# Performance work log

Measured on AMD Instinct MI355X. Metric: run time of the kernel, lower is better.

The kernel has to match this reference:

```python
import jax, jax.numpy as jnp
import numpy as np

N_NODES = 100000


def _aggregate(features, edge_index, edge_weight):
    # weighted scatter-add over edges + degree normalization (clamped at 1)
    src = edge_index[0]
    dst = edge_index[1]
    w = edge_weight  # [E]
    msgs = features[src] * w[:, None]                      # [E, D]
    agg = jax.ops.segment_sum(msgs, dst, num_segments=N_NODES)   # [N, D]
    deg = jax.ops.segment_sum(w, dst, num_segments=N_NODES)      # [N]
    deg = jnp.maximum(deg, 1.0)
    return agg / deg[:, None]


def setup_inputs() -> dict:
    key = jax.random.key(0)
    k1, k2, k3, k4, k5, k6, k7, k8, k9 = jax.random.split(key, 9)
    input_dim, hidden_dim, embedding_dim, num_classes = 128, 128, 64, 40
    E = 1600000
    node_features = jax.random.normal(k1, (N_NODES, input_dim), dtype=jnp.float32)
    edge_index = jax.random.randint(k2, (2, E), 0, N_NODES, dtype=jnp.int64)
    edge_weight = jax.random.uniform(k3, (E,), dtype=jnp.float32)
    s1 = 1.0 / np.sqrt(input_dim)
    s2 = 1.0 / np.sqrt(hidden_dim)
    s3 = 1.0 / np.sqrt(embedding_dim)
    W1 = jax.random.uniform(k4, (hidden_dim, input_dim), minval=-s1, maxval=s1, dtype=jnp.float32)
    b1 = jax.random.uniform(k5, (hidden_dim,), minval=-s1, maxval=s1, dtype=jnp.float32)
    W2 = jax.random.uniform(k6, (embedding_dim, hidden_dim), minval=-s2, maxval=s2, dtype=jnp.float32)
    b2 = jax.random.uniform(k7, (embedding_dim,), minval=-s2, maxval=s2, dtype=jnp.float32)
    W3 = jax.random.uniform(k8, (num_classes, embedding_dim), minval=-s3, maxval=s3, dtype=jnp.float32)
    b3 = jax.random.uniform(k9, (num_classes,), minval=-s3, maxval=s3, dtype=jnp.float32)
    return {"node_features": node_features, "edge_index": edge_index, "edge_weight": edge_weight,
            "W1": W1, "b1": b1, "W2": W2, "b2": b2, "W3": W3, "b3": b3}


def reference(node_features, edge_index, edge_weight, W1, b1, W2, b2, W3, b3):
    hidden = _aggregate(node_features, edge_index, edge_weight)
    hidden = jax.nn.relu(hidden @ W1.T + b1)
    embedding = _aggregate(hidden, edge_index, edge_weight) @ W2.T + b2
    logits = embedding @ W3.T + b3
    return (embedding, logits)
```

## Files before the change

### kernel.cpp

```cpp
#include <hip/hip_runtime.h>
#include <cstddef>

#define DIM 128
#define DH 64
#define NC 40
#define NBLKA 1024
#define BKT 512

typedef short bf16x8 __attribute__((ext_vector_type(8)));
typedef float f32x4  __attribute__((ext_vector_type(4)));

__device__ __forceinline__ unsigned short f2bf(float f) {
    unsigned int u = __float_as_uint(f);
    u += 0x7FFFu + ((u >> 16) & 1u);
    return (unsigned short)(u >> 16);
}
__device__ __forceinline__ float bf2f(unsigned short h) {
    return __uint_as_float(((unsigned int)h) << 16);
}

__global__ __launch_bounds__(256) void kA1(
    const int* __restrict__ dstv, int E, int CHUNK,
    int* __restrict__ cnt , int NBbkt,
    const float* __restrict__ W1, const float* __restrict__ W2,
    unsigned short* __restrict__ W1bf, unsigned short* __restrict__ W2bf)
{
    int b = blockIdx.x;
    if (b < NBLKA) {
        __shared__ int h[256];
        for (int i = threadIdx.x; i < 256; i += 256) h[i] = 0;
        __syncthreads();
        int lo = b * CHUNK, hi = min(E, lo + CHUNK);
        for (int e = lo + threadIdx.x; e < hi; e += 256)
            atomicAdd(&h[dstv[e] >> 9], 1);
        __syncthreads();
        for (int i = threadIdx.x; i < NBbkt; i += 256)
            cnt[(size_t)b * NBbkt + i] = h[i];
    } else {
        int i = (b - NBLKA) * 256 + threadIdx.x;
        if (i < DIM * DIM) W1bf[i] = f2bf(W1[i]);
        else if (i < DIM * DIM + DH * DIM) {
            int j = i - DIM * DIM;
            W2bf[j] = f2bf(W2[j]);
        }
    }
}

__global__ __launch_bounds__(256) void kA2a(
    int* __restrict__ cnt , int* __restrict__ total, int NBbkt)
{
    __shared__ int wsum[4];
    int b = blockIdx.x;
    int t = threadIdx.x;
    int v[4]; int s = 0;
    #pragma unroll
    for (int i = 0; i < 4; ++i) { v[i] = cnt[(size_t)(4 * t + i) * NBbkt + b]; s += v[i]; }
    int lane = t & 63, wv = t >> 6;
    int si = s;
    #pragma unroll
    for (int off = 1; off < 64; off <<= 1) {
        int x = __shfl_up(si, off);
        if (lane >= off) si += x;
    }
    if (lane == 63) wsum[wv] = si;
    __syncthreads();
    int wbase = 0;
    for (int i = 0; i < wv; ++i) wbase += wsum[i];
    int run = wbase + si - s;
    #pragma unroll
    for (int i = 0; i < 4; ++i) { cnt[(size_t)(4 * t + i) * NBbkt + b] = run; run += v[i]; }
    if (t == 255) total[b] = run;
}

__global__ __launch_bounds__(256) void kA2b(
    const int* __restrict__ total, int* __restrict__ bucketBase, int NBbkt)
{
    __shared__ int wsum[4];
    int t = threadIdx.x;
    int v = (t < NBbkt) ? total[t] : 0;
    int lane = t & 63, wv = t >> 6;
    int si = v;
    #pragma unroll
    for (int off = 1; off < 64; off <<= 1) {
        int x = __shfl_up(si, off);
        if (lane >= off) si += x;
    }
    if (lane == 63) wsum[wv] = si;
    __syncthreads();
    int wbase = 0;
    for (int i = 0; i < wv; ++i) wbase += wsum[i];
    int incl = wbase + si;
    if (t < NBbkt) bucketBase[t + 1] = incl;
    if (t == 0) bucketBase[0] = 0;
}

__global__ __launch_bounds__(256) void kA3(
    const int* __restrict__ srcv, const int* __restrict__ dstv,
    const float* __restrict__ wv_, int E, int CHUNK,
    const int* __restrict__ exclOff, const int* __restrict__ bucketBase,
    uint2* __restrict__ staging, int NBbkt,
    const float4* __restrict__ feat4, ushort4* __restrict__ featbf4, int n8)
{
    int b = blockIdx.x;
    if (b < NBLKA) {
        __shared__ int cur[256];
        for (int i = threadIdx.x; i < NBbkt; i += 256)
            cur[i] = bucketBase[i] + exclOff[(size_t)b * NBbkt + i];
        __syncthreads();
        int lo = b * CHUNK, hi = min(E, lo + CHUNK);
        for (int e = lo + threadIdx.x; e < hi; e += 256) {
            int d = dstv[e];
            unsigned q = (unsigned)(wv_[e] * 32767.f + 0.5f);
            unsigned word = (q << 17) | (unsigned)srcv[e];
            int pos = atomicAdd(&cur[d >> 9], 1);
            staging[pos] = make_uint2(word, (unsigned)(d & (BKT - 1)));
        }
    } else {
        int i = (b - NBLKA) * 256 + threadIdx.x;
        if (i < n8) {
            float4 x = feat4[2 * i], y = feat4[2 * i + 1];
            ushort4 o1, o2;
            o1.x = f2bf(x.x); o1.y = f2bf(x.y); o1.z = f2bf(x.z); o1.w = f2bf(x.w);
            o2.x = f2bf(y.x); o2.y = f2bf(y.y); o2.z = f2bf(y.z); o2.w = f2bf(y.w);
            featbf4[2 * i] = o1; featbf4[2 * i + 1] = o2;
        }
    }
}

__global__ __launch_bounds__(256) void kB(
    const uint2* __restrict__ staging, const int* __restrict__ bucketBase,
    unsigned* __restrict__ csr, int* __restrict__ row_start, int n)
{
    __shared__ int bins[BKT];
    __shared__ int cur[BKT];
    __shared__ int wsum[4];
    int b = blockIdx.x;
    int base = bucketBase[b], cntE = bucketBase[b + 1] - base;
    int t = threadIdx.x;
    for (int i = t; i < BKT; i += 256) bins[i] = 0;
    __syncthreads();
    for (int i = t; i < cntE; i += 256)
        atomicAdd(&bins[staging[base + i].y], 1);
    __syncthreads();
    int b0 = bins[2 * t], b1 = bins[2 * t + 1];
    int s = b0 + b1;
    int lane = t & 63, wv = t >> 6;
    int si = s;
    #pragma unroll
    for (int off = 1; off < 64; off <<= 1) {
        int x = __shfl_up(si, off);
        if (lane >= off) si += x;
    }
    if (lane == 63) wsum[wv] = si;
    __syncthreads();
    int wbase = 0;
    for (int i = 0; i < wv; ++i) wbase += wsum[i];
    int excl = wbase + si - s;
    int v0 = b * BKT + 2 * t;
    if (v0 <= n)     row_start[v0]     = base + excl;
    if (v0 + 1 <= n) row_start[v0 + 1] = base + excl + b0;
    cur[2 * t]     = base + excl;
    cur[2 * t + 1] = base + excl + b0;
    __syncthreads();
    for (int i = t; i < cntE; i += 256) {
        uint2 r = staging[base + i];
        int pos = atomicAdd(&cur[r.y], 1);
        csr[pos] = r.x;
    }
}

__global__ __launch_bounds__(256) void k_gather1(
    const unsigned short* __restrict__ feat, const int* __restrict__ row_start,
    const unsigned* __restrict__ csr, float* __restrict__ deg,
    unsigned short* __restrict__ aggbf, int n)
{
    constexpr int G = 16, EPW = 4;
    int lane = threadIdx.x & 63;
    int q    = lane & (G - 1);
    int sub  = lane / G;
    int wid  = (int)((blockIdx.x * blockDim.x + threadIdx.x) >> 6);
    int nw   = (int)((gridDim.x * blockDim.x) >> 6);
    for (int v = wid; v < n; v += nw) {
        int beg = row_start[v], end = row_start[v + 1];
        float acc[8];
        #pragma unroll
        for (int e = 0; e < 8; ++e) acc[e] = 0.f;
        float dsum = 0.f;
        for (int b = beg; b < end; b += 64) {
            int cnt = end - b; if (cnt > 64) cnt = 64;
            unsigned word = (lane < cnt) ? csr[b + lane] : 0u;
            dsum += (float)(word >> 17) * (1.f / 32767.f);
            int iters = (cnt + EPW - 1) / EPW;
            for (int j = 0; j < iters; ++j) {
                unsigned wj = (unsigned)__shfl((int)word, j * EPW + sub);
                int   s   = (int)(wj & 0x1FFFFu);
                float wgt = (float)(wj >> 17) * (1.f / 32767.f);
                bf16x8 f = *(const bf16x8*)(feat + (size_t)s * DIM + q * 8);
                #pragma unroll
                for (int e = 0; e < 8; ++e)
                    acc[e] += wgt * bf2f((unsigned short)f[e]);
            }
        }
        #pragma unroll
        for (int m = 32; m >= G; m >>= 1)
            #pragma unroll
            for (int e = 0; e < 8; ++e) acc[e] += __shfl_xor(acc[e], m);
        #pragma unroll
        for (int m = 32; m >= 1; m >>= 1) dsum += __shfl_xor(dsum, m);
        if (lane == 0) deg[v] = dsum;
        float dg = dsum > 1.f ? dsum : 1.f;
        float inv = 1.f / dg;
        if (lane < G) {
            bf16x8 o;
            #pragma unroll
            for (int e = 0; e < 8; ++e) o[e] = (short)f2bf(acc[e] * inv);
            int p = q ^ (v & 7);
            *(bf16x8*)(aggbf + (size_t)v * DIM + p * 8) = o;
        }
    }
}

__global__ __launch_bounds__(256) void k_gather2(
    const unsigned short* __restrict__ Zbf, const int* __restrict__ row_start,
    const unsigned* __restrict__ csr, const float* __restrict__ deg,
    const float* __restrict__ b2, float* __restrict__ out_emb, int n)
{
    constexpr int G = 8, EPW = 8;
    int lane = threadIdx.x & 63;
    int q    = lane & (G - 1);
    int sub  = lane / G;
    int wid  = (int)((blockIdx.x * blockDim.x + threadIdx.x) >> 6);
    int nw   = (int)((gridDim.x * blockDim.x) >> 6);
    for (int v = wid; v < n; v += nw) {
        int beg = row_start[v], end = row_start[v + 1];
        float acc[8];
        #pragma unroll
        for (int e = 0; e < 8; ++e) acc[e] = 0.f;
        for (int b = beg; b < end; b += 64) {
            int cnt = end - b; if (cnt > 64) cnt = 64;
            unsigned word = (lane < cnt) ? csr[b + lane] : 0u;
            int iters = (cnt + EPW - 1) / EPW;
            for (int j = 0; j < iters; ++j) {
                unsigned wj = (unsigned)__shfl((int)word, j * EPW + sub);
                int   s   = (int)(wj & 0x1FFFFu);
                float wgt = (float)(wj >> 17) * (1.f / 32767.f);
                bf16x8 f = *(const bf16x8*)(Zbf + (size_t)s * DH + q * 8);
                #pragma unroll
                for (int e = 0; e < 8; ++e)
                    acc[e] += wgt * bf2f((unsigned short)f[e]);
            }
        }
        #pragma unroll
        for (int m = 32; m >= G; m >>= 1)
            #pragma unroll
            for (int e = 0; e < 8; ++e) acc[e] += __shfl_xor(acc[e], m);
        if (lane < G) {
            float dg = deg[v]; dg = dg > 1.f ? dg : 1.f;
            float inv = 1.f / dg;
            const float4* b2p = (const float4*)(b2 + q * 8);
            float4 ba = b2p[0], bb = b2p[1];
            float4* dst = (float4*)(out_emb + (size_t)v * DH + q * 8);
            dst[0] = make_float4(acc[0]*inv + ba.x, acc[1]*inv + ba.y,
                                 acc[2]*inv + ba.z, acc[3]*inv + ba.w);
            dst[1] = make_float4(acc[4]*inv + bb.x, acc[5]*inv + bb.y,
                                 acc[6]*inv + bb.z, acc[7]*inv + bb.w);
        }
    }
}

__global__ __launch_bounds__(256) void k_dense1z(
    const unsigned short* __restrict__ aggbf,
    const unsigned short* __restrict__ W1bf, const float* __restrict__ b1,
    const unsigned short* __restrict__ W2bf,
    unsigned short* __restrict__ Zbf, int n)
{
    __shared__ unsigned short sAgg[64 * 128];
    __shared__ unsigned short sW1[128 * 128];
    __shared__ unsigned short sW2[64 * 128];
    __shared__ unsigned short sHid[64 * 128];
    int t = threadIdx.x;
    int lane = t & 63;
    int w = t >> 6;
    int row0 = (int)blockIdx.x * 64;

    #pragma unroll
    for (int i = 0; i < 4; ++i) {
        int B = t + 256 * i;
        int r = B >> 4, p = B & 15;
        *(bf16x8*)&sAgg[r * 128 + p * 8] =
            *(const bf16x8*)(aggbf + (size_t)(row0 + r) * DIM + p * 8);
    }
    #pragma unroll
    for (int i = 0; i < 8; ++i) {
        int B = t + 256 * i;
        int r = B >> 4, q = B & 15;
        bf16x8 v = *(const bf16x8*)(W1bf + r * 128 + q * 8);
        *(bf16x8*)&sW1[r * 128 + ((q ^ (r & 7)) * 8)] = v;
    }
    #pragma unroll
    for (int i = 0; i < 4; ++i) {
        int B = t + 256 * i;
        int r = B >> 4, q = B & 15;
        bf16x8 v = *(const bf16x8*)(W2bf + r * 128 + q * 8);
        *(bf16x8*)&sW2[r * 128 + ((q ^ (r & 7)) * 8)] = v;
    }
    __syncthreads();

    int c = lane & 15;
    int g = lane >> 4;
    int ar = 16 * w + c;

    bf16x8 a1[4];
    #pragma unroll
    for (int ks = 0; ks < 4; ++ks) {
        int q = ks * 4 + g;
        a1[ks] = *(const bf16x8*)&sAgg[ar * 128 + ((q ^ (ar & 7)) * 8)];
    }
    f32x4 acc[8];
    #pragma unroll
    for (int nt = 0; nt < 8; ++nt) {
        float bv = b1[nt * 16 + c];
        acc[nt] = (f32x4){bv, bv, bv, bv};
    }
    #pragma unroll
    for (int ks = 0; ks < 4; ++ks) {
        #pragma unroll
        for (int nt = 0; nt < 8; ++nt) {
            int rn = nt * 16 + c;
            int q = ks * 4 + g;
            bf16x8 b = *(const bf16x8*)&sW1[rn * 128 + ((q ^ (rn & 7)) * 8)];
            acc[nt] = __builtin_amdgcn_mfma_f32_16x16x32_bf16(a1[ks], b, acc[nt], 0, 0, 0);
        }
    }
    #pragma unroll
    for (int nt = 0; nt < 8; ++nt) {
        #pragma unroll
        for (int rg = 0; rg < 4; ++rg) {
            float v = acc[nt][rg];
            v = v > 0.f ? v : 0.f;
            int hr = 16 * w + 4 * g + rg;
            int col = nt * 16 + c;
            int qq = col >> 3, oo = col & 7;
            sHid[hr * 128 + ((qq ^ (hr & 7)) * 8) + oo] = f2bf(v);
        }
    }
    __syncthreads();

    bf16x8 a2[4];
    #pragma unroll
    for (int ks = 0; ks < 4; ++ks) {
        int q = ks * 4 + g;
        a2[ks] = *(const bf16x8*)&sHid[ar * 128 + ((q ^ (ar & 7)) * 8)];
    }
    f32x4 acc2[4];
    #pragma unroll
    for (int nt = 0; nt < 4; ++nt) acc2[nt] = (f32x4){0.f, 0.f, 0.f, 0.f};
    #pragma unroll
    for (int ks = 0; ks < 4; ++ks) {
        #pragma unroll
        for (int nt = 0; nt < 4; ++nt) {
            int rn = nt * 16 + c;
            int q = ks * 4 + g;
            bf16x8 b = *(const bf16x8*)&sW2[rn * 128 + ((q ^ (rn & 7)) * 8)];
            acc2[nt] = __builtin_amdgcn_mfma_f32_16x16x32_bf16(a2[ks], b, acc2[nt], 0, 0, 0);
        }
    }
    #pragma unroll
    for (int nt = 0; nt < 4; ++nt) {
        #pragma unroll
        for (int rg = 0; rg < 4; ++rg) {
            int m = row0 + 16 * w + 4 * g + rg;
            if (m < n) Zbf[(size_t)m * DH + nt * 16 + c] = f2bf(acc2[nt][rg]);
        }
    }
}

__global__ __launch_bounds__(256) void k_out(
    const float* __restrict__ emb, const float* __restrict__ W3,
    const float* __restrict__ b3, float* __restrict__ out_log, int n)
{
    __shared__ float sE[16 * 68];
    __shared__ float sW3[NC * 68];
    int t = threadIdx.x;
    int row0 = (int)blockIdx.x * 16;

    for (int i = t; i < NC * DH; i += 256) {
        int cc = i >> 6, k = i & 63;
        sW3[cc * 68 + k] = W3[i];
    }
    for (int i = t; i < 16 * DH; i += 256) {
        int r = i >> 6, k = i & 63;
        int row = row0 + r;
        sE[r * 68 + k] = (row < n) ? emb[(size_t)row * DH + k] : 0.f;
    }
    __syncthreads();

    for (int idx = t; idx < 16 * NC; idx += 256) {
        int r = idx / NC, cc = idx % NC;
        int row = row0 + r;
        if (row >= n) continue;
        float acc = b3[cc];
        #pragma unroll 8
        for (int k = 0; k < DH; ++k)
            acc += sE[r * 68 + k] * sW3[cc * 68 + k];
        out_log[(size_t)row * NC + cc] = acc;
    }
}

extern "C" void kernel_launch(void* const* d_in, const int* in_sizes, int n_in,
                              void* d_out, int out_size, void* d_ws, size_t ws_size,
                              hipStream_t stream)
{
    const float* feat = (const float*)d_in[0];
    const int*   eidx = (const int*)d_in[1];
    const float* ew   = (const float*)d_in[2];
    const float* W1   = (const float*)d_in[3];
    const float* b1   = (const float*)d_in[4];
    const float* W2   = (const float*)d_in[5];
    const float* b2   = (const float*)d_in[6];
    const float* W3   = (const float*)d_in[7];
    const float* b3   = (const float*)d_in[8];

    int E = in_sizes[2];
    int n = in_sizes[0] / DIM;
    int npad = (n + 63) & ~63;
    int NBbkt = (n + BKT - 1) / BKT;
    int CHUNK = (E + NBLKA - 1) / NBLKA;

    const int* srcv = eidx;
    const int* dstv = eidx + E;

    float* out_emb = (float*)d_out;
    float* out_log = out_emb + (size_t)n * DH;

    size_t nf = (size_t)n * DIM;

    char* wsb = (char*)d_ws;
    size_t off = 0;
    auto alloc = [&](size_t bytes) -> void* {
        void* p = wsb + off;
        off = (off + bytes + 255) & ~(size_t)255;
        return p;
    };
    unsigned short* aggbf   = (unsigned short*)alloc((size_t)npad * DIM * 2);
    unsigned short* Zbf     = (unsigned short*)alloc((size_t)npad * DH * 2);
    unsigned short* featbf  = (unsigned short*)alloc(nf * 2);
    unsigned short* W1bf    = (unsigned short*)alloc((size_t)DIM * DIM * 2);
    unsigned short* W2bf    = (unsigned short*)alloc((size_t)DH * DIM * 2);
    float*          deg     = (float*)alloc((size_t)n * 4);
    int*            row_start = (int*)alloc((size_t)(n + 1) * 4);
    unsigned*       csr     = (unsigned*)alloc((size_t)E * 4);
    uint2*          staging = (uint2*)alloc((size_t)E * 8);
    int*            cnt     = (int*)alloc((size_t)NBLKA * NBbkt * 4);
    int*            total   = (int*)alloc((size_t)NBbkt * 4);
    int*            bucketBase = (int*)alloc((size_t)(NBbkt + 1) * 4);

    int WB = (DIM * DIM + DH * DIM + 255) / 256;
    kA1<<<NBLKA + WB, 256, 0, stream>>>(dstv, E, CHUNK, cnt, NBbkt, W1, W2, W1bf, W2bf);
    kA2a<<<NBbkt, 256, 0, stream>>>(cnt, total, NBbkt);
    kA2b<<<1, 256, 0, stream>>>(total, bucketBase, NBbkt);
    int n8 = (int)(nf / 8);
    int FB = (n8 + 255) / 256;
    kA3<<<NBLKA + FB, 256, 0, stream>>>(srcv, dstv, ew, E, CHUNK, cnt, bucketBase,
                                        staging, NBbkt, (const float4*)feat,
                                        (ushort4*)featbf, n8);
    kB<<<NBbkt, 256, 0, stream>>>(staging, bucketBase, csr, row_start, n);

    int gblk = (n + 3) / 4;
    k_gather1<<<gblk, 256, 0, stream>>>(featbf, row_start, csr, deg, aggbf, n);
    k_dense1z<<<npad / 64, 256, 0, stream>>>(aggbf, W1bf, b1, W2bf, Zbf, n);
    k_gather2<<<gblk, 256, 0, stream>>>(Zbf, row_start, csr, deg, b2, out_emb, n);
    k_out<<<(n + 15) / 16, 256, 0, stream>>>(out_emb, W3, b3, out_log, n);
}
```

Measured before the change: 321.6 us.

## Fuse logits projection into gather2, persist dense kernel, vectorize edge passes

Removes the separate k_out kernel by computing the W3 projection inside k_gather2 straight from the in-register embedding, with W3 staged in shared memory per block. This avoids re-reading the embedding and saves one launch. k_dense1z becomes a persistent kernel capped at 512 blocks, so the W1/W2 shared-memory staging is amortized across many 64-row tiles. The histogram and scatter passes now read edges four at a time with int4/float4 loads, and CHUNK is rounded to a multiple of 4 to keep those loads aligned. The costs are W3 staging in every gather2 block (gblk is about 25k blocks) and fewer concurrent blocks for the dense kernel.

Result: slower. 351.4 us (+9.2%).

```diff
diff --git a/kernel.cpp b/kernel.cpp
--- a/kernel.cpp
+++ b/kernel.cpp
@@ -31,8 +31,17 @@
         for (int i = threadIdx.x; i < 256; i += 256) h[i] = 0;
         __syncthreads();
         int lo = b * CHUNK, hi = min(E, lo + CHUNK);
-        for (int e = lo + threadIdx.x; e < hi; e += 256)
-            atomicAdd(&h[dstv[e] >> 9], 1);
+        for (int e0 = lo + 4 * threadIdx.x; e0 < hi; e0 += 1024) {
+            if (e0 + 4 <= hi) {
+                int4 d4 = *(const int4*)(dstv + e0);
+                atomicAdd(&h[d4.x >> 9], 1);
+                atomicAdd(&h[d4.y >> 9], 1);
+                atomicAdd(&h[d4.z >> 9], 1);
+                atomicAdd(&h[d4.w >> 9], 1);
+            } else {
+                for (int e = e0; e < hi; ++e) atomicAdd(&h[dstv[e] >> 9], 1);
+            }
+        }
         __syncthreads();
         for (int i = threadIdx.x; i < NBbkt; i += 256)
             cnt[(size_t)b * NBbkt + i] = h[i];
@@ -108,12 +117,30 @@
             cur[i] = bucketBase[i] + exclOff[(size_t)b * NBbkt + i];
         __syncthreads();
         int lo = b * CHUNK, hi = min(E, lo + CHUNK);
-        for (int e = lo + threadIdx.x; e < hi; e += 256) {
-            int d = dstv[e];
-            unsigned q = (unsigned)(wv_[e] * 32767.f + 0.5f);
-            unsigned word = (q << 17) | (unsigned)srcv[e];
-            int pos = atomicAdd(&cur[d >> 9], 1);
-            staging[pos] = make_uint2(word, (unsigned)(d & (BKT - 1)));
+        for (int e0 = lo + 4 * threadIdx.x; e0 < hi; e0 += 1024) {
+            if (e0 + 4 <= hi) {
+                int4   d4 = *(const int4*)(dstv + e0);
+                int4   s4 = *(const int4*)(srcv + e0);
+                float4 w4 = *(const float4*)(wv_ + e0);
+                int dd[4] = {d4.x, d4.y, d4.z, d4.w};
+                int ss[4] = {s4.x, s4.y, s4.z, s4.w};
+                float ww[4] = {w4.x, w4.y, w4.z, w4.w};
+                #pragma unroll
+                for (int i = 0; i < 4; ++i) {
+                    unsigned q = (unsigned)(ww[i] * 32767.f + 0.5f);
+                    unsigned word = (q << 17) | (unsigned)ss[i];
+                    int pos = atomicAdd(&cur[dd[i] >> 9], 1);
+                    staging[pos] = make_uint2(word, (unsigned)(dd[i] & (BKT - 1)));
+                }
+            } else {
+                for (int e = e0; e < hi; ++e) {
+                    int d = dstv[e];
+                    unsigned q = (unsigned)(wv_[e] * 32767.f + 0.5f);
+                    unsigned word = (q << 17) | (unsigned)srcv[e];
+                    int pos = atomicAdd(&cur[d >> 9], 1);
+                    staging[pos] = make_uint2(word, (unsigned)(d & (BKT - 1)));
+                }
+            }
         }
     } else {
         int i = (b - NBLKA) * 256 + threadIdx.x;
@@ -220,16 +247,29 @@
     }
 }
 
+#define SW3P 66
 __global__ __launch_bounds__(256) void k_gather2(
     const unsigned short* __restrict__ Zbf, const int* __restrict__ row_start,
     const unsigned* __restrict__ csr, const float* __restrict__ deg,
-    const float* __restrict__ b2, float* __restrict__ out_emb, int n)
-{
+    const float* __restrict__ b2, const float* __restrict__ W3,
+    const float* __restrict__ b3,
+    float* __restrict__ out_emb, float* __restrict__ out_log, int n)
+{
+    __shared__ float sW3[NC * SW3P];
+    __shared__ float sb3[NC];
     constexpr int G = 8, EPW = 8;
-    int lane = threadIdx.x & 63;
+    int t = threadIdx.x;
+    for (int i = t; i < NC * DH; i += 256) {
+        int cc = i >> 6, k = i & 63;
+        sW3[cc * SW3P + k] = W3[i];
+    }
+    if (t < NC) sb3[t] = b3[t];
+    __syncthreads();
+
+    int lane = t & 63;
     int q    = lane & (G - 1);
-    int sub  = lane / G;
-    int wid  = (int)((blockIdx.x * blockDim.x + threadIdx.x) >> 6);
+    int sub  = lane >> 3;
+    int wid  = (int)((blockIdx.x * blockDim.x + t) >> 6);
     int nw   = (int)((gridDim.x * blockDim.x) >> 6);
     for (int v = wid; v < n; v += nw) {
         int beg = row_start[v], end = row_start[v + 1];
@@ -254,16 +294,39 @@
         for (int m = 32; m >= G; m >>= 1)
             #pragma unroll
             for (int e = 0; e < 8; ++e) acc[e] += __shfl_xor(acc[e], m);
+
+        float dg = deg[v]; dg = dg > 1.f ? dg : 1.f;
+        float inv = 1.f / dg;
+        float emb[8];
+        #pragma unroll
+        for (int e = 0; e < 8; ++e) emb[e] = acc[e] * inv + b2[q * 8 + e];
+
         if (lane < G) {
-            float dg = deg[v]; dg = dg > 1.f ? dg : 1.f;
-            float inv = 1.f / dg;
-            const float4* b2p = (const float4*)(b2 + q * 8);
-            float4 ba = b2p[0], bb = b2p[1];
             float4* dst = (float4*)(out_emb + (size_t)v * DH + q * 8);
-            dst[0] = make_float4(acc[0]*inv + ba.x, acc[1]*inv + ba.y,
-                                 acc[2]*inv + ba.z, acc[3]*inv + ba.w);
-            dst[1] = make_float4(acc[4]*inv + bb.x, acc[5]*inv + bb.y,
-                                 acc[6]*inv + bb.z, acc[7]*inv + bb.w);
+            dst[0] = make_float4(emb[0], emb[1], emb[2], emb[3]);
+            dst[1] = make_float4(emb[4], emb[5], emb[6], emb[7]);
+        }
+
+        float part[5];
+        #pragma unroll
+        for (int j = 0; j < 5; ++j) {
+            int c = sub * 5 + j;
+            const float* wrow = &sW3[c * SW3P + q * 8];
+            float p = 0.f;
+            #pragma unroll
+            for (int e = 0; e < 8; ++e) p += emb[e] * wrow[e];
+            part[j] = p;
+        }
+        #pragma unroll
+        for (int m = 1; m <= 4; m <<= 1)
+            #pragma unroll
+            for (int j = 0; j < 5; ++j) part[j] += __shfl_xor(part[j], m);
+        if (q == 0) {
+            #pragma unroll
+            for (int j = 0; j < 5; ++j) {
+                int c = sub * 5 + j;
+                out_log[(size_t)v * NC + c] = part[j] + sb3[c];
+            }
         }
     }
 }
@@ -272,7 +335,7 @@
     const unsigned short* __restrict__ aggbf,
     const unsigned short* __restrict__ W1bf, const float* __restrict__ b1,
     const unsigned short* __restrict__ W2bf,
-    unsigned short* __restrict__ Zbf, int n)
+    unsigned short* __restrict__ Zbf, int n, int ntiles)
 {
     __shared__ unsigned short sAgg[64 * 128];
     __shared__ unsigned short sW1[128 * 128];
@@ -281,15 +344,7 @@
     int t = threadIdx.x;
     int lane = t & 63;
     int w = t >> 6;
-    int row0 = (int)blockIdx.x * 64;
-
-    #pragma unroll
-    for (int i = 0; i < 4; ++i) {
-        int B = t + 256 * i;
-        int r = B >> 4, p = B & 15;
-        *(bf16x8*)&sAgg[r * 128 + p * 8] =
-            *(const bf16x8*)(aggbf + (size_t)(row0 + r) * DIM + p * 8);
-    }
+
     #pragma unroll
     for (int i = 0; i < 8; ++i) {
         int B = t + 256 * i;
@@ -304,106 +359,87 @@
         bf16x8 v = *(const bf16x8*)(W2bf + r * 128 + q * 8);
         *(bf16x8*)&sW2[r * 128 + ((q ^ (r & 7)) * 8)] = v;
     }
-    __syncthreads();
 
     int c = lane & 15;
     int g = lane >> 4;
     int ar = 16 * w + c;
-
-    bf16x8 a1[4];
-    #pragma unroll
-    for (int ks = 0; ks < 4; ++ks) {
-        int q = ks * 4 + g;
-        a1[ks] = *(const bf16x8*)&sAgg[ar * 128 + ((q ^ (ar & 7)) * 8)];
-    }
-    f32x4 acc[8];
-    #pragma unroll
-    for (int nt = 0; nt < 8; ++nt) {
-        float bv = b1[nt * 16 + c];
-        acc[nt] = (f32x4){bv, bv, bv, bv};
-    }
-    #pragma unroll
-    for (int ks = 0; ks < 4; ++ks) {
+    float b1v[8];
+    #pragma unroll
+    for (int nt = 0; nt < 8; ++nt) b1v[nt] = b1[nt * 16 + c];
+
+    for (int tile = blockIdx.x; tile < ntiles; tile += gridDim.x) {
+        int row0 = tile * 64;
+        #pragma unroll
+        for (int i = 0; i < 4; ++i) {
+            int B = t + 256 * i;
+            int r = B >> 4, p = B & 15;
+            *(bf16x8*)&sAgg[r * 128 + p * 8] =
+                *(const bf16x8*)(aggbf + (size_t)(row0 + r) * DIM + p * 8);
+        }
+        __syncthreads();
+
+        bf16x8 a1[4];
+        #pragma unroll
+        for (int ks = 0; ks < 4; ++ks) {
+            int q = ks * 4 + g;
+            a1[ks] = *(const bf16x8*)&sAgg[ar * 128 + ((q ^ (ar & 7)) * 8)];
+        }
+        f32x4 acc[8];
+        #pragma unroll
+        for (int nt = 0; nt < 8; ++nt)
+            acc[nt] = (f32x4){b1v[nt], b1v[nt], b1v[nt], b1v[nt]};
+        #pragma unroll
+        for (int ks = 0; ks < 4; ++ks) {
+            #pragma unroll
+            for (int nt = 0; nt < 8; ++nt) {
+                int rn = nt * 16 + c;
+                int q = ks * 4 + g;
+                bf16x8 b = *(const bf16x8*)&sW1[rn * 128 + ((q ^ (rn & 7)) * 8)];
+                acc[nt] = __builtin_amdgcn_mfma_f32_16x16x32_bf16(a1[ks], b, acc[nt], 0, 0, 0);
+            }
+        }
         #pragma unroll
         for (int nt = 0; nt < 8; ++nt) {
-            int rn = nt * 16 + c;
+            #pragma unroll
+            for (int rg = 0; rg < 4; ++rg) {
+                float v = acc[nt][rg];
+                v = v > 0.f ? v : 0.f;
+                int hr = 16 * w + 4 * g + rg;
+                int col = nt * 16 + c;
+                int qq = col >> 3, oo = col & 7;
+                sHid[hr * 128 + ((qq ^ (hr & 7)) * 8) + oo] = f2bf(v);
+            }
+        }
+        __syncthreads();
+
+        bf16x8 a2[4];
+        #pragma unroll
+        for (int ks = 0; ks < 4; ++ks) {
             int q = ks * 4 + g;
-            bf16x8 b = *(const bf16x8*)&sW1[rn * 128 + ((q ^ (rn & 7)) * 8)];
-            acc[nt] = __builtin_amdgcn_mfma_f32_16x16x32_bf16(a1[ks], b, acc[nt], 0, 0, 0);
-        }
-    }
-    #pragma unroll
-    for (int nt = 0; nt < 8; ++nt) {
-        #pragma unroll
-        for (int rg = 0; rg < 4; ++rg) {
-            float v = acc[nt][rg];
-            v = v > 0.f ? v : 0.f;
-            int hr = 16 * w + 4 * g + rg;
-            int col = nt * 16 + c;
-            int qq = col >> 3, oo = col & 7;
-            sHid[hr * 128 + ((qq ^ (hr & 7)) * 8) + oo] = f2bf(v);
-        }
-    }
-    __syncthreads();
-
-    bf16x8 a2[4];
-    #pragma unroll
-    for (int ks = 0; ks < 4; ++ks) {
-        int q = ks * 4 + g;
-        a2[ks] = *(const bf16x8*)&sHid[ar * 128 + ((q ^ (ar & 7)) * 8)];
-    }
-    f32x4 acc2[4];
-    #pragma unroll
-    for (int nt = 0; nt < 4; ++nt) acc2[nt] = (f32x4){0.f, 0.f, 0.f, 0.f};
-    #pragma unroll
-    for (int ks = 0; ks < 4; ++ks) {
+            a2[ks] = *(const bf16x8*)&sHid[ar * 128 + ((q ^ (ar & 7)) * 8)];
+        }
+        f32x4 acc2[4];
+        #pragma unroll
+        for (int nt = 0; nt < 4; ++nt) acc2[nt] = (f32x4){0.f, 0.f, 0.f, 0.f};
+        #pragma unroll
+        for (int ks = 0; ks < 4; ++ks) {
+            #pragma unroll
+            for (int nt = 0; nt < 4; ++nt) {
+                int rn = nt * 16 + c;
+                int q = ks * 4 + g;
+                bf16x8 b = *(const bf16x8*)&sW2[rn * 128 + ((q ^ (rn & 7)) * 8)];
+                acc2[nt] = __builtin_amdgcn_mfma_f32_16x16x32_bf16(a2[ks], b, acc2[nt], 0, 0, 0);
+            }
+        }
         #pragma unroll
         for (int nt = 0; nt < 4; ++nt) {
-            int rn = nt * 16 + c;
-            int q = ks * 4 + g;
-            bf16x8 b = *(const bf16x8*)&sW2[rn * 128 + ((q ^ (rn & 7)) * 8)];
-            acc2[nt] = __builtin_amdgcn_mfma_f32_16x16x32_bf16(a2[ks], b, acc2[nt], 0, 0, 0);
-        }
-    }
-    #pragma unroll
-    for (int nt = 0; nt < 4; ++nt) {
-        #pragma unroll
-        for (int rg = 0; rg < 4; ++rg) {
-            int m = row0 + 16 * w + 4 * g + rg;
-            if (m < n) Zbf[(size_t)m * DH + nt * 16 + c] = f2bf(acc2[nt][rg]);
-        }
-    }
-}
-
-__global__ __launch_bounds__(256) void k_out(
-    const float* __restrict__ emb, const float* __restrict__ W3,
-    const float* __restrict__ b3, float* __restrict__ out_log, int n)
-{
-    __shared__ float sE[16 * 68];
-    __shared__ float sW3[NC * 68];
-    int t = threadIdx.x;
-    int row0 = (int)blockIdx.x * 16;
-
-    for (int i = t; i < NC * DH; i += 256) {
-        int cc = i >> 6, k = i & 63;
-        sW3[cc * 68 + k] = W3[i];
-    }
-    for (int i = t; i < 16 * DH; i += 256) {
-        int r = i >> 6, k = i & 63;
-        int row = row0 + r;
-        sE[r * 68 + k] = (row < n) ? emb[(size_t)row * DH + k] : 0.f;
-    }
-    __syncthreads();
-
-    for (int idx = t; idx < 16 * NC; idx += 256) {
-        int r = idx / NC, cc = idx % NC;
-        int row = row0 + r;
-        if (row >= n) continue;
-        float acc = b3[cc];
-        #pragma unroll 8
-        for (int k = 0; k < DH; ++k)
-            acc += sE[r * 68 + k] * sW3[cc * 68 + k];
-        out_log[(size_t)row * NC + cc] = acc;
+            #pragma unroll
+            for (int rg = 0; rg < 4; ++rg) {
+                int m = row0 + 16 * w + 4 * g + rg;
+                if (m < n) Zbf[(size_t)m * DH + nt * 16 + c] = f2bf(acc2[nt][rg]);
+            }
+        }
+        __syncthreads();
     }
 }
 
@@ -425,7 +461,7 @@
     int n = in_sizes[0] / DIM;
     int npad = (n + 63) & ~63;
     int NBbkt = (n + BKT - 1) / BKT;
-    int CHUNK = (E + NBLKA - 1) / NBLKA;
+    int CHUNK = (((E + NBLKA - 1) / NBLKA) + 3) & ~3;
 
     const int* srcv = eidx;
     const int* dstv = eidx + E;
@@ -468,7 +504,9 @@
 
     int gblk = (n + 3) / 4;
     k_gather1<<<gblk, 256, 0, stream>>>(featbf, row_start, csr, deg, aggbf, n);
-    k_dense1z<<<npad / 64, 256, 0, stream>>>(aggbf, W1bf, b1, W2bf, Zbf, n);
-    k_gather2<<<gblk, 256, 0, stream>>>(Zbf, row_start, csr, deg, b2, out_emb, n);
-    k_out<<<(n + 15) / 16, 256, 0, stream>>>(out_emb, W3, b3, out_log, n);
-}
+    int ntiles = npad / 64;
+    int pgrid = ntiles < 512 ? ntiles : 512;
+    k_dense1z<<<pgrid, 256, 0, stream>>>(aggbf, W1bf, b1, W2bf, Zbf, n, ntiles);
+    k_gather2<<<gblk, 256, 0, stream>>>(Zbf, row_start, csr, deg, b2, W3, b3,
+                                        out_emb, out_log, n);
+}
```
